# Performance work log

Measured on AMD Instinct MI355X. Metric: run time of the kernel, lower is better.

Reference implementation:

```python
import jax, jax.numpy as jnp
import numpy as np

HIDDEN = 2048
NUM_HEADS = 16
HEAD_DIM = 128
WINDOW_SIZE = 512
NUM_GLOBAL = 16
SCALING = HEAD_DIM ** -0.5


def setup_inputs() -> dict:
    key = jax.random.key(0)
    ks = jax.random.split(key, 5)
    std = HIDDEN ** -0.5
    hidden_states = jax.random.normal(ks[0], (1, 4096, HIDDEN), dtype=jnp.float32)
    # Linear weights stored as (in, out) so y = x @ W
    Wq = jax.random.normal(ks[1], (HIDDEN, NUM_HEADS * HEAD_DIM), dtype=jnp.float32) * std
    Wk = jax.random.normal(ks[2], (HIDDEN, NUM_HEADS * HEAD_DIM), dtype=jnp.float32) * std
    Wv = jax.random.normal(ks[3], (HIDDEN, NUM_HEADS * HEAD_DIM), dtype=jnp.float32) * std
    Wo = jax.random.normal(ks[4], (NUM_HEADS * HEAD_DIM, HIDDEN), dtype=jnp.float32) * std
    return {"hidden_states": hidden_states, "Wq": Wq, "Wk": Wk, "Wv": Wv, "Wo": Wo}


def _sliding_mask(q_len: int, kv_len: int) -> jnp.ndarray:
    q_pos = jnp.arange(q_len)[:, None]
    kv_pos = jnp.arange(kv_len)[None, :]
    half_window = WINDOW_SIZE // 2
    local = jnp.abs(q_pos - kv_pos) < half_window
    glob = (q_pos < NUM_GLOBAL) | (kv_pos < NUM_GLOBAL)
    mask = local | glob
    return jnp.where(mask, 0.0, -jnp.inf).astype(jnp.float32)


def reference(hidden_states, Wq, Wk, Wv, Wo):
    bsz, q_len, _ = hidden_states.shape
    q = (hidden_states @ Wq).reshape(bsz, q_len, NUM_HEADS, HEAD_DIM).transpose(0, 2, 1, 3)
    k = (hidden_states @ Wk).reshape(bsz, q_len, NUM_HEADS, HEAD_DIM).transpose(0, 2, 1, 3)
    v = (hidden_states @ Wv).reshape(bsz, q_len, NUM_HEADS, HEAD_DIM).transpose(0, 2, 1, 3)
    mask = _sliding_mask(q_len, q_len)[None, None]  # [1,1,S,S]
    scores = jnp.einsum("bhqd,bhkd->bhqk", q, k) * SCALING + mask
    attn = jax.nn.softmax(scores.astype(jnp.float32), axis=-1).astype(q.dtype)
    out = jnp.einsum("bhqk,bhkd->bhqd", attn, v)
    out = out.transpose(0, 2, 1, 3).reshape(bsz, q_len, NUM_HEADS * HEAD_DIM)
    return out @ Wo
```

## Files before the change

### kernel.cpp

```cpp
#include <hip/hip_runtime.h>
#include <stdint.h>

#define SEQ    4096
#define HID    2048
#define NQKV   6144
#define QKW    4096
#define NH     16
#define HD     128
#define SCALE  0.08838834764831845f
#define GQC    32

typedef unsigned short u16;
typedef __attribute__((ext_vector_type(8))) short bf16x8;
typedef __attribute__((ext_vector_type(4))) float f32x4;

__device__ __forceinline__ u16 f2bf(float f) {
  union { float f; unsigned u; } v; v.f = f;
  unsigned r = v.u + 0x7FFFu + ((v.u >> 16) & 1u);
  return (u16)(r >> 16);
}

__device__ __forceinline__ float bf2f(u16 b) {
  union { unsigned u; float f; } c; c.u = ((unsigned)b) << 16; return c.f;
}

__device__ __forceinline__ void async16(const u16* g, u16* l) {
  __builtin_amdgcn_global_load_lds(
      (const __attribute__((address_space(1))) unsigned int*)g,
      (__attribute__((address_space(3))) unsigned int*)l, 16, 0, 0);
}

__global__ __launch_bounds__(256) void cvt_f32_bf16(const float* __restrict__ in,
                                                    u16* __restrict__ out, int n4) {
  int i = blockIdx.x * 256 + threadIdx.x;
  if (i >= n4) return;
  float4 v = ((const float4*)in)[i];
  ushort4 o;
  o.x = f2bf(v.x); o.y = f2bf(v.y); o.z = f2bf(v.z); o.w = f2bf(v.w);
  ((ushort4*)out)[i] = o;
}

__global__ __launch_bounds__(256) void transpose_w4(const float* __restrict__ W0,
                                                    const float* __restrict__ W1,
                                                    const float* __restrict__ W2,
                                                    const float* __restrict__ W3,
                                                    u16* __restrict__ Wcat,
                                                    u16* __restrict__ Wot) {
  __shared__ __align__(16) u16 Ts[64 * 68];
  const int n0 = blockIdx.x * 64;
  const int k0 = blockIdx.y * 64;
  const int z = blockIdx.z;
  const float* W = (z == 0) ? W0 : (z == 1) ? W1 : (z == 2) ? W2 : W3;
  u16* Wt = (z < 3) ? (Wcat + (size_t)z * 2048 * 2048) : Wot;
  const int t = threadIdx.x;
#pragma unroll
  for (int p = 0; p < 4; ++p) {
    int f = (t + p * 256) * 4;
    int r = f >> 6, c = f & 63;
    float4 v = *(const float4*)&W[(size_t)(k0 + r) * 2048 + n0 + c];
    ushort4 o; o.x = f2bf(v.x); o.y = f2bf(v.y); o.z = f2bf(v.z); o.w = f2bf(v.w);
    *(ushort4*)&Ts[r * 68 + c] = o;
  }
  __syncthreads();
#pragma unroll
  for (int p = 0; p < 4; ++p) {
    int g = (t + p * 256) * 4;
    int r = g >> 6, c = g & 63;
    ushort4 o;
    o.x = Ts[(c + 0) * 68 + r];
    o.y = Ts[(c + 1) * 68 + r];
    o.z = Ts[(c + 2) * 68 + r];
    o.w = Ts[(c + 3) * 68 + r];
    *(ushort4*)&Wt[(size_t)(n0 + r) * 2048 + k0 + c] = o;
  }
}

template <typename OutT, bool WVT>
__global__ __launch_bounds__(256) void gemm_bt(const u16* __restrict__ A,
                                               const u16* __restrict__ B,
                                               OutT* __restrict__ C,
                                               u16* __restrict__ VTout,
                                               int K, int ldc) {
  __shared__ __align__(16) u16 As[128 * 32];
  __shared__ __align__(16) u16 Bs[128 * 32];
  const int m0 = blockIdx.y * 128;
  const int n0 = blockIdx.x * 128;
  const int tid = threadIdx.x;
  const int wid = tid >> 6;
  const int lane = tid & 63;
  const int wm = wid & 1, wn = wid >> 1;
  const int l15 = lane & 15, g4 = lane >> 4;

  const int srow = wid * 32 + (lane >> 2);
  const int scol = (lane & 3) * 8;

  f32x4 acc[4][4] = {};

  const u16* pa0 = &A[(size_t)(m0 + srow) * K + scol];
  const u16* pa1 = &A[(size_t)(m0 + srow + 16) * K + scol];
  const u16* pb0 = &B[(size_t)(n0 + srow) * K + scol];
  const u16* pb1 = &B[(size_t)(n0 + srow + 16) * K + scol];
  u16* la0 = &As[(wid * 32) * 32];
  u16* la1 = &As[(wid * 32 + 16) * 32];
  u16* lb0 = &Bs[(wid * 32) * 32];
  u16* lb1 = &Bs[(wid * 32 + 16) * 32];

  for (int kt = 0; kt < K; kt += 32) {
    __syncthreads();
    async16(pa0 + kt, la0);
    async16(pa1 + kt, la1);
    async16(pb0 + kt, lb0);
    async16(pb1 + kt, lb1);
    __syncthreads();
    bf16x8 af[4], bfr[4];
#pragma unroll
    for (int i = 0; i < 4; ++i)
      af[i] = *(const bf16x8*)&As[(wm * 64 + i * 16 + l15) * 32 + g4 * 8];
#pragma unroll
    for (int i = 0; i < 4; ++i)
      bfr[i] = *(const bf16x8*)&Bs[(wn * 64 + i * 16 + l15) * 32 + g4 * 8];
#pragma unroll
    for (int mi = 0; mi < 4; ++mi)
#pragma unroll
      for (int ni = 0; ni < 4; ++ni)
        acc[mi][ni] = __builtin_amdgcn_mfma_f32_16x16x32_bf16(af[mi], bfr[ni], acc[mi][ni], 0, 0, 0);
  }

  if (WVT && n0 >= QKW) {
#pragma unroll
    for (int mi = 0; mi < 4; ++mi)
#pragma unroll
      for (int ni = 0; ni < 4; ++ni) {
        const int nv = n0 - QKW + wn * 64 + ni * 16 + l15;
        const int hh = nv >> 7, dd = nv & 127;
        u16* base = &VTout[((size_t)hh * HD + dd) * SEQ];
        const int mb = m0 + wm * 64 + mi * 16 + g4 * 4;
        u16 pk[4];
#pragma unroll
        for (int r = 0; r < 4; ++r) pk[r] = f2bf(acc[mi][ni][r]);
        *(uint2*)&base[mb] = *(uint2*)pk;
      }
  } else {
#pragma unroll
    for (int mi = 0; mi < 4; ++mi)
#pragma unroll
      for (int ni = 0; ni < 4; ++ni) {
        const int n = n0 + wn * 64 + ni * 16 + l15;
#pragma unroll
        for (int r = 0; r < 4; ++r) {
          const int m = m0 + wm * 64 + mi * 16 + g4 * 4 + r;
          float v = acc[mi][ni][r];
          if constexpr (sizeof(OutT) == 2) {
            C[(size_t)m * ldc + n] = (OutT)f2bf(v);
          } else {
            C[(size_t)m * ldc + n] = v;
          }
        }
      }
  }
}

__global__ __launch_bounds__(256, 3) void attn_kernel(const u16* __restrict__ qk,
                                                      const u16* __restrict__ vt,
                                                      u16* __restrict__ out) {
  __shared__ __align__(16) u16 Ks[64 * 128];
  __shared__ __align__(16) u16 VTs[128 * 64];
  __shared__ __align__(16) u16 Ps[64 * 64];
  const int q0 = blockIdx.x * 64;
  const int h = blockIdx.y;
  const int tid = threadIdx.x;
  const int w = tid >> 6;
  const int lane = tid & 63;
  const int l15 = lane & 15, g4 = lane >> 4;
  const int l7 = l15 & 7;

  bf16x8 qf[4];
  {
    const u16* qrow = &qk[(size_t)(q0 + w * 16 + l15) * QKW + h * HD + g4 * 8];
#pragma unroll
    for (int kk = 0; kk < 4; ++kk) qf[kk] = *(const bf16x8*)&qrow[kk * 32];
  }

  float m_run = -1e30f, l_run = 0.f;
  f32x4 o[8] = {};

  int lo = q0 - 255;
  int lo_blk = (lo < 0) ? 0 : (lo >> 6);
  int hi_blk = (q0 + 318) >> 6;
  if (hi_blk > 63) hi_blk = 63;
  const int extra = (lo_blk > 0) ? 1 : 0;
  const int nsteps = hi_blk - lo_blk + 1 + extra;

  for (int step = 0; step < nsteps; ++step) {
    const int kb = (extra && step == 0) ? 0 : (lo_blk + step - extra);
    const int kv0 = kb * 64;
    __syncthreads();
#pragma unroll
    for (int p = 0; p < 4; ++p) {
      int id = p * 256 + tid;
      int r = id >> 4, c8 = id & 15;
      uint4 v = *(const uint4*)&qk[(size_t)(kv0 + r) * QKW + 2048 + h * HD + c8 * 8];
      *(uint4*)&Ks[r * 128 + ((c8 ^ (r & 15)) * 8)] = v;
    }
#pragma unroll
    for (int p = 0; p < 4; ++p) {
      int id = p * 256 + tid;
      int r = id >> 3, c8 = id & 7;
      uint4 v = *(const uint4*)&vt[(size_t)h * (HD * SEQ) + (size_t)r * SEQ + kv0 + c8 * 8];
      *(uint4*)&VTs[r * 64 + ((c8 ^ (r & 7)) * 8)] = v;
    }
    __syncthreads();

    f32x4 st[4] = {};
#pragma unroll
    for (int kk = 0; kk < 4; ++kk) {
#pragma unroll
      for (int t4 = 0; t4 < 4; ++t4) {
        bf16x8 ak = *(const bf16x8*)&Ks[(t4 * 16 + l15) * 128 + (((kk * 4 + g4) ^ l15) * 8)];
        st[t4] = __builtin_amdgcn_mfma_f32_16x16x32_bf16(ak, qf[kk], st[t4], 0, 0, 0);
      }
    }

    const int q = q0 + w * 16 + l15;
    float pv[4][4];
    float cmax = -1e30f;
#pragma unroll
    for (int t4 = 0; t4 < 4; ++t4)
#pragma unroll
      for (int r = 0; r < 4; ++r) {
        int kv = kv0 + t4 * 16 + g4 * 4 + r;
        int dq = q - kv; if (dq < 0) dq = -dq;
        bool ok = (dq < 256) || (kv < 16);
        float s = ok ? st[t4][r] * SCALE : -1e30f;
        pv[t4][r] = s;
        cmax = fmaxf(cmax, s);
      }
    cmax = fmaxf(cmax, __shfl_xor(cmax, 16, 64));
    cmax = fmaxf(cmax, __shfl_xor(cmax, 32, 64));
    float mnew = fmaxf(m_run, cmax);
    float csum = 0.f;
#pragma unroll
    for (int t4 = 0; t4 < 4; ++t4)
#pragma unroll
      for (int r = 0; r < 4; ++r) {
        float p = __expf(pv[t4][r] - mnew);
        pv[t4][r] = p;
        csum += p;
      }
    csum += __shfl_xor(csum, 16, 64);
    csum += __shfl_xor(csum, 32, 64);
    float alpha = __expf(m_run - mnew);
    m_run = mnew;
    l_run = l_run * alpha + csum;

#pragma unroll
    for (int t4 = 0; t4 < 4; ++t4) {
      u16 pk[4];
#pragma unroll
      for (int r = 0; r < 4; ++r) pk[r] = f2bf(pv[t4][r]);
      int c8 = t4 * 2 + (g4 >> 1);
      *(uint2*)&Ps[(w * 16 + l15) * 64 + ((c8 ^ l7) * 8) + (g4 & 1) * 4] = *(uint2*)pk;
    }

    float al[4];
#pragma unroll
    for (int r = 0; r < 4; ++r) al[r] = __shfl(alpha, g4 * 4 + r, 64);
#pragma unroll
    for (int nt = 0; nt < 8; ++nt)
#pragma unroll
      for (int r = 0; r < 4; ++r) o[nt][r] *= al[r];

#pragma unroll
    for (int ks = 0; ks < 2; ++ks) {
      bf16x8 ap = *(const bf16x8*)&Ps[(w * 16 + l15) * 64 + (((ks * 4 + g4) ^ l7) * 8)];
#pragma unroll
      for (int nt = 0; nt < 8; ++nt) {
        bf16x8 bv = *(const bf16x8*)&VTs[(nt * 16 + l15) * 64 + (((ks * 4 + g4) ^ l7) * 8)];
        o[nt] = __builtin_amdgcn_mfma_f32_16x16x32_bf16(ap, bv, o[nt], 0, 0, 0);
      }
    }
  }

  float lr[4];
#pragma unroll
  for (int r = 0; r < 4; ++r) lr[r] = 1.f / __shfl(l_run, g4 * 4 + r, 64);
#pragma unroll
  for (int nt = 0; nt < 8; ++nt)
#pragma unroll
    for (int r = 0; r < 4; ++r) {
      const int m = q0 + w * 16 + g4 * 4 + r;
      if (m < 16) continue;
      const int n = h * HD + nt * 16 + l15;
      out[(size_t)m * HID + n] = f2bf(o[nt][r] * lr[r]);
    }
}

__global__ __launch_bounds__(256) void attn_global(const u16* __restrict__ qk,
                                                   const u16* __restrict__ vt,
                                                   float* __restrict__ Opart,
                                                   float* __restrict__ MLpart) {
  __shared__ __align__(16) u16 Ks[64 * 136];
  __shared__ __align__(16) u16 Vs[64 * 136];
  const int chunk = blockIdx.x, h = blockIdx.y;
  const int t = threadIdx.x;
  const int q = t >> 4, dg = t & 15;

  float qr[8];
  {
    bf16x8 v = *(const bf16x8*)&qk[(size_t)q * QKW + h * HD + dg * 8];
#pragma unroll
    for (int j = 0; j < 8; ++j) qr[j] = bf2f((u16)v[j]);
  }
  float m_run = -1e30f, l_run = 0.f, o[8] = {};
  const int kvbase = chunk * (SEQ / GQC);

  for (int st = 0; st < (SEQ / GQC) / 64; ++st) {
    const int kv0 = kvbase + st * 64;
    __syncthreads();
#pragma unroll
    for (int p = 0; p < 4; ++p) {
      int f = (t + p * 256) * 8;
      int r = f >> 7, c = f & 127;
      *(uint4*)&Ks[r * 136 + c] = *(const uint4*)&qk[(size_t)(kv0 + r) * QKW + 2048 + h * HD + c];
    }
#pragma unroll
    for (int p = 0; p < 4; ++p) {
      int id = p * 256 + t;
      int d = id >> 3, c8 = id & 7;
      uint4 v = *(const uint4*)&vt[(size_t)h * (HD * SEQ) + (size_t)d * SEQ + kv0 + c8 * 8];
      const u16* pv16 = (const u16*)&v;
#pragma unroll
      for (int j = 0; j < 8; ++j) Vs[(c8 * 8 + j) * 136 + d] = pv16[j];
    }
    __syncthreads();
    for (int kv = 0; kv < 64; ++kv) {
      bf16x8 kr = *(const bf16x8*)&Ks[kv * 136 + dg * 8];
      float s = 0.f;
#pragma unroll
      for (int j = 0; j < 8; ++j) s += qr[j] * bf2f((u16)kr[j]);
      s += __shfl_xor(s, 1, 64); s += __shfl_xor(s, 2, 64);
      s += __shfl_xor(s, 4, 64); s += __shfl_xor(s, 8, 64);
      s *= SCALE;
      float mnew = fmaxf(m_run, s);
      float alpha = __expf(m_run - mnew);
      float p = __expf(s - mnew);
      m_run = mnew;
      l_run = l_run * alpha + p;
      bf16x8 vr = *(const bf16x8*)&Vs[kv * 136 + dg * 8];
#pragma unroll
      for (int j = 0; j < 8; ++j) o[j] = o[j] * alpha + p * bf2f((u16)vr[j]);
    }
  }
  float* op = &Opart[(((size_t)h * GQC + chunk) * 16 + q) * HD + dg * 8];
#pragma unroll
  for (int j = 0; j < 8; ++j) op[j] = o[j];
  if (dg == 0) {
    float* ml = &MLpart[(((size_t)h * GQC + chunk) * 16 + q) * 2];
    ml[0] = m_run; ml[1] = l_run;
  }
}

__global__ __launch_bounds__(256) void attn_gred(const float* __restrict__ Opart,
                                                 const float* __restrict__ MLpart,
                                                 u16* __restrict__ out) {
  const int h = blockIdx.x;
  const int t = threadIdx.x;
  const int q = t >> 4, dg = t & 15;
  float M = -1e30f;
  for (int c = 0; c < GQC; ++c)
    M = fmaxf(M, MLpart[(((size_t)h * GQC + c) * 16 + q) * 2]);
  float L = 0.f, o[8] = {};
  for (int c = 0; c < GQC; ++c) {
    const float* ml = &MLpart[(((size_t)h * GQC + c) * 16 + q) * 2];
    float e = __expf(ml[0] - M);
    L += e * ml[1];
    const float* op = &Opart[(((size_t)h * GQC + c) * 16 + q) * HD + dg * 8];
#pragma unroll
    for (int j = 0; j < 8; ++j) o[j] += e * op[j];
  }
  float inv = 1.f / L;
  u16 tmp[8];
#pragma unroll
  for (int j = 0; j < 8; ++j) tmp[j] = f2bf(o[j] * inv);
  *(uint4*)&out[(size_t)q * HID + h * HD + dg * 8] = *(uint4*)tmp;
}

extern "C" void kernel_launch(void* const* d_in, const int* in_sizes, int n_in,
                              void* d_out, int out_size, void* d_ws, size_t ws_size,
                              hipStream_t stream) {
  const float* X  = (const float*)d_in[0];
  const float* Wq = (const float*)d_in[1];
  const float* Wk = (const float*)d_in[2];
  const float* Wv = (const float*)d_in[3];
  const float* Wo = (const float*)d_in[4];
  float* out = (float*)d_out;

  char* ws = (char*)d_ws;
  u16* Xbf    = (u16*)(ws);
  u16* Wcat   = (u16*)(ws + (size_t)(16 << 20));
  u16* AttnO  = (u16*)(ws + (size_t)(16 << 20));
  float* Opart  = (float*)(ws + (size_t)(32 << 20));
  float* MLpart = (float*)(ws + (size_t)(36 << 20));
  u16* QK     = (u16*)(ws + (size_t)(40 << 20));
  u16* VT     = (u16*)(ws + (size_t)(72 << 20));
  u16* Wot    = (u16*)(ws + (size_t)(88 << 20));

  cvt_f32_bf16<<<dim3(8192), dim3(256), 0, stream>>>(X, Xbf, (SEQ * HID) / 4);
  transpose_w4<<<dim3(32, 32, 4), 256, 0, stream>>>(Wq, Wk, Wv, Wo, Wcat, Wot);
  gemm_bt<u16, true><<<dim3(48, 32), 256, 0, stream>>>(Xbf, Wcat, QK, VT, HID, QKW);
  attn_global<<<dim3(GQC, NH), 256, 0, stream>>>(QK, VT, Opart, MLpart);
  attn_kernel<<<dim3(64, 16), 256, 0, stream>>>(QK, VT, AttnO);
  attn_gred<<<dim3(NH), 256, 0, stream>>>(Opart, MLpart, AttnO);
  gemm_bt<float, false><<<dim3(16, 32), 256, 0, stream>>>(AttnO, Wot, out, nullptr, HID, HID);
}
```

Baseline: 431.9 us.

## Process 128 queries per attention block with async K/V loads

The sliding-window attention kernel now handles 128 queries per block, two 16-row query slices per wave, so each K and V tile staged in shared memory serves twice as many queries. Global-to-LDS copies switch to async16 with the XOR swizzle applied on the source address. The PV MFMA operand order is swapped so each lane keeps a whole query row. That removes the alpha/l shuffles and allows 8-byte vectorized output stores. The cost is more registers, a minimum of 2 waves per SIMD instead of 3, fewer blocks in the grid, and slightly more wasted masked KV tiles per block.

```diff
diff --git a/kernel.cpp b/kernel.cpp
--- a/kernel.cpp
+++ b/kernel.cpp
@@ -160,33 +160,33 @@
   }
 }
 
-__global__ __launch_bounds__(256, 3) void attn_kernel(const u16* __restrict__ qk,
+__global__ __launch_bounds__(256, 2) void attn_kernel(const u16* __restrict__ qk,
                                                       const u16* __restrict__ vt,
                                                       u16* __restrict__ out) {
   __shared__ __align__(16) u16 Ks[64 * 128];
   __shared__ __align__(16) u16 VTs[128 * 64];
-  __shared__ __align__(16) u16 Ps[64 * 64];
-  const int q0 = blockIdx.x * 64;
+  __shared__ __align__(16) u16 Ps[128 * 64];
+  const int q0 = blockIdx.x * 128;
   const int h = blockIdx.y;
   const int tid = threadIdx.x;
   const int w = tid >> 6;
   const int lane = tid & 63;
-  const int l15 = lane & 15, g4 = lane >> 4;
-  const int l7 = l15 & 7;
-
-  bf16x8 qf[4];
-  {
-    const u16* qrow = &qk[(size_t)(q0 + w * 16 + l15) * QKW + h * HD + g4 * 8];
-#pragma unroll
-    for (int kk = 0; kk < 4; ++kk) qf[kk] = *(const bf16x8*)&qrow[kk * 32];
-  }
-
-  float m_run = -1e30f, l_run = 0.f;
-  f32x4 o[8] = {};
+  const int l15 = lane & 15, g4 = lane >> 4, l7 = lane & 7;
+
+  bf16x8 qf[2][4];
+#pragma unroll
+  for (int qs = 0; qs < 2; ++qs) {
+    const u16* qrow = &qk[(size_t)(q0 + w * 32 + qs * 16 + l15) * QKW + h * HD + g4 * 8];
+#pragma unroll
+    for (int kk = 0; kk < 4; ++kk) qf[qs][kk] = *(const bf16x8*)&qrow[kk * 32];
+  }
+
+  float m_run[2] = {-1e30f, -1e30f}, l_run[2] = {0.f, 0.f};
+  f32x4 o[2][8] = {};
 
   int lo = q0 - 255;
   int lo_blk = (lo < 0) ? 0 : (lo >> 6);
-  int hi_blk = (q0 + 318) >> 6;
+  int hi_blk = (q0 + 382) >> 6;
   if (hi_blk > 63) hi_blk = 63;
   const int extra = (lo_blk > 0) ? 1 : 0;
   const int nsteps = hi_blk - lo_blk + 1 + extra;
@@ -197,102 +197,108 @@
     __syncthreads();
 #pragma unroll
     for (int p = 0; p < 4; ++p) {
-      int id = p * 256 + tid;
-      int r = id >> 4, c8 = id & 15;
-      uint4 v = *(const uint4*)&qk[(size_t)(kv0 + r) * QKW + 2048 + h * HD + c8 * 8];
-      *(uint4*)&Ks[r * 128 + ((c8 ^ (r & 15)) * 8)] = v;
+      const int r = w * 16 + p * 4 + (lane >> 4);
+      const u16* src = &qk[(size_t)(kv0 + r) * QKW + 2048 + h * HD + (((lane & 15) ^ (r & 15)) * 8)];
+      async16(src, &Ks[(w * 16 + p * 4) * 128]);
     }
 #pragma unroll
     for (int p = 0; p < 4; ++p) {
-      int id = p * 256 + tid;
-      int r = id >> 3, c8 = id & 7;
-      uint4 v = *(const uint4*)&vt[(size_t)h * (HD * SEQ) + (size_t)r * SEQ + kv0 + c8 * 8];
-      *(uint4*)&VTs[r * 64 + ((c8 ^ (r & 7)) * 8)] = v;
-    }
-    __syncthreads();
-
-    f32x4 st[4] = {};
+      const int r = w * 32 + p * 8 + (lane >> 3);
+      const u16* src = &vt[(size_t)h * (HD * SEQ) + (size_t)r * SEQ + kv0 + (((lane & 7) ^ (r & 7)) * 8)];
+      async16(src, &VTs[(w * 32 + p * 8) * 64]);
+    }
+    __syncthreads();
+
+    f32x4 st[2][4] = {};
 #pragma unroll
     for (int kk = 0; kk < 4; ++kk) {
+      bf16x8 ak[4];
+#pragma unroll
+      for (int t4 = 0; t4 < 4; ++t4)
+        ak[t4] = *(const bf16x8*)&Ks[(t4 * 16 + l15) * 128 + (((kk * 4 + g4) ^ l15) * 8)];
+#pragma unroll
+      for (int qs = 0; qs < 2; ++qs)
+#pragma unroll
+        for (int t4 = 0; t4 < 4; ++t4)
+          st[qs][t4] = __builtin_amdgcn_mfma_f32_16x16x32_bf16(ak[t4], qf[qs][kk], st[qs][t4], 0, 0, 0);
+    }
+
+#pragma unroll
+    for (int qs = 0; qs < 2; ++qs) {
+      const int q = q0 + w * 32 + qs * 16 + l15;
+      float cmax = -1e30f;
+#pragma unroll
+      for (int t4 = 0; t4 < 4; ++t4)
+#pragma unroll
+        for (int r = 0; r < 4; ++r) {
+          int kv = kv0 + t4 * 16 + g4 * 4 + r;
+          int dq = q - kv; if (dq < 0) dq = -dq;
+          bool ok = (dq < 256) || (kv < 16);
+          float s = ok ? st[qs][t4][r] * SCALE : -1e30f;
+          st[qs][t4][r] = s;
+          cmax = fmaxf(cmax, s);
+        }
+      cmax = fmaxf(cmax, __shfl_xor(cmax, 16, 64));
+      cmax = fmaxf(cmax, __shfl_xor(cmax, 32, 64));
+      float mnew = fmaxf(m_run[qs], cmax);
+      float csum = 0.f;
+#pragma unroll
+      for (int t4 = 0; t4 < 4; ++t4)
+#pragma unroll
+        for (int r = 0; r < 4; ++r) {
+          float p = __expf(st[qs][t4][r] - mnew);
+          st[qs][t4][r] = p;
+          csum += p;
+        }
+      csum += __shfl_xor(csum, 16, 64);
+      csum += __shfl_xor(csum, 32, 64);
+      float a = __expf(m_run[qs] - mnew);
+      m_run[qs] = mnew;
+      l_run[qs] = l_run[qs] * a + csum;
+
 #pragma unroll
       for (int t4 = 0; t4 < 4; ++t4) {
-        bf16x8 ak = *(const bf16x8*)&Ks[(t4 * 16 + l15) * 128 + (((kk * 4 + g4) ^ l15) * 8)];
-        st[t4] = __builtin_amdgcn_mfma_f32_16x16x32_bf16(ak, qf[kk], st[t4], 0, 0, 0);
+        u16 pk[4];
+#pragma unroll
+        for (int r = 0; r < 4; ++r) pk[r] = f2bf(st[qs][t4][r]);
+        int c8 = t4 * 2 + (g4 >> 1);
+        *(uint2*)&Ps[(w * 32 + qs * 16 + l15) * 64 + ((c8 ^ l7) * 8) + (g4 & 1) * 4] = *(uint2*)pk;
       }
-    }
-
-    const int q = q0 + w * 16 + l15;
-    float pv[4][4];
-    float cmax = -1e30f;
-#pragma unroll
-    for (int t4 = 0; t4 < 4; ++t4)
-#pragma unroll
-      for (int r = 0; r < 4; ++r) {
-        int kv = kv0 + t4 * 16 + g4 * 4 + r;
-        int dq = q - kv; if (dq < 0) dq = -dq;
-        bool ok = (dq < 256) || (kv < 16);
-        float s = ok ? st[t4][r] * SCALE : -1e30f;
-        pv[t4][r] = s;
-        cmax = fmaxf(cmax, s);
-      }
-    cmax = fmaxf(cmax, __shfl_xor(cmax, 16, 64));
-    cmax = fmaxf(cmax, __shfl_xor(cmax, 32, 64));
-    float mnew = fmaxf(m_run, cmax);
-    float csum = 0.f;
-#pragma unroll
-    for (int t4 = 0; t4 < 4; ++t4)
-#pragma unroll
-      for (int r = 0; r < 4; ++r) {
-        float p = __expf(pv[t4][r] - mnew);
-        pv[t4][r] = p;
-        csum += p;
-      }
-    csum += __shfl_xor(csum, 16, 64);
-    csum += __shfl_xor(csum, 32, 64);
-    float alpha = __expf(m_run - mnew);
-    m_run = mnew;
-    l_run = l_run * alpha + csum;
-
-#pragma unroll
-    for (int t4 = 0; t4 < 4; ++t4) {
-      u16 pk[4];
-#pragma unroll
-      for (int r = 0; r < 4; ++r) pk[r] = f2bf(pv[t4][r]);
-      int c8 = t4 * 2 + (g4 >> 1);
-      *(uint2*)&Ps[(w * 16 + l15) * 64 + ((c8 ^ l7) * 8) + (g4 & 1) * 4] = *(uint2*)pk;
-    }
-
-    float al[4];
-#pragma unroll
-    for (int r = 0; r < 4; ++r) al[r] = __shfl(alpha, g4 * 4 + r, 64);
-#pragma unroll
-    for (int nt = 0; nt < 8; ++nt)
-#pragma unroll
-      for (int r = 0; r < 4; ++r) o[nt][r] *= al[r];
+#pragma unroll
+      for (int nt = 0; nt < 8; ++nt)
+#pragma unroll
+        for (int r = 0; r < 4; ++r) o[qs][nt][r] *= a;
+    }
 
 #pragma unroll
     for (int ks = 0; ks < 2; ++ks) {
-      bf16x8 ap = *(const bf16x8*)&Ps[(w * 16 + l15) * 64 + (((ks * 4 + g4) ^ l7) * 8)];
+      bf16x8 ap[2];
+#pragma unroll
+      for (int qs = 0; qs < 2; ++qs)
+        ap[qs] = *(const bf16x8*)&Ps[(w * 32 + qs * 16 + l15) * 64 + (((ks * 4 + g4) ^ l7) * 8)];
 #pragma unroll
       for (int nt = 0; nt < 8; ++nt) {
         bf16x8 bv = *(const bf16x8*)&VTs[(nt * 16 + l15) * 64 + (((ks * 4 + g4) ^ l7) * 8)];
-        o[nt] = __builtin_amdgcn_mfma_f32_16x16x32_bf16(ap, bv, o[nt], 0, 0, 0);
+#pragma unroll
+        for (int qs = 0; qs < 2; ++qs)
+          o[qs][nt] = __builtin_amdgcn_mfma_f32_16x16x32_bf16(bv, ap[qs], o[qs][nt], 0, 0, 0);
       }
     }
   }
 
-  float lr[4];
-#pragma unroll
-  for (int r = 0; r < 4; ++r) lr[r] = 1.f / __shfl(l_run, g4 * 4 + r, 64);
-#pragma unroll
-  for (int nt = 0; nt < 8; ++nt)
-#pragma unroll
-    for (int r = 0; r < 4; ++r) {
-      const int m = q0 + w * 16 + g4 * 4 + r;
-      if (m < 16) continue;
-      const int n = h * HD + nt * 16 + l15;
-      out[(size_t)m * HID + n] = f2bf(o[nt][r] * lr[r]);
-    }
+#pragma unroll
+  for (int qs = 0; qs < 2; ++qs) {
+    if (q0 + w * 32 + qs * 16 < 16) continue;
+    const int q = q0 + w * 32 + qs * 16 + l15;
+    const float inv = 1.f / l_run[qs];
+#pragma unroll
+    for (int nt = 0; nt < 8; ++nt) {
+      u16 pk[4];
+#pragma unroll
+      for (int r = 0; r < 4; ++r) pk[r] = f2bf(o[qs][nt][r] * inv);
+      *(uint2*)&out[(size_t)q * HID + h * HD + nt * 16 + g4 * 4] = *(uint2*)pk;
+    }
+  }
 }
 
 __global__ __launch_bounds__(256) void attn_global(const u16* __restrict__ qk,
@@ -409,7 +415,7 @@
   transpose_w4<<<dim3(32, 32, 4), 256, 0, stream>>>(Wq, Wk, Wv, Wo, Wcat, Wot);
   gemm_bt<u16, true><<<dim3(48, 32), 256, 0, stream>>>(Xbf, Wcat, QK, VT, HID, QKW);
   attn_global<<<dim3(GQC, NH), 256, 0, stream>>>(QK, VT, Opart, MLpart);
-  attn_kernel<<<dim3(64, 16), 256, 0, stream>>>(QK, VT, AttnO);
+  attn_kernel<<<dim3(SEQ / 128, NH), 256, 0, stream>>>(QK, VT, AttnO);
   attn_gred<<<dim3(NH), 256, 0, stream>>>(Opart, MLpart, AttnO);
   gemm_bt<float, false><<<dim3(16, 32), 256, 0, stream>>>(AttnO, Wot, out, nullptr, HID, HID);
 }
```

After: 431.2 us. No clear change (-0.2%).
